# Performance work log

Hardware: AMD Instinct MI355X
Metric: run time of the kernel (lower is better)

## Reference

```python
import jax, jax.numpy as jnp
import numpy as np

S, I, C_M, C_P, C_Z = 128, 384, 256, 32, 128

def setup_inputs() -> dict:
    key = jax.random.key(0)
    ks = jax.random.split(key, 7)
    sc = 1.0 / np.sqrt(C_M)
    return {
        "msa_rep": jax.random.normal(ks[0], (S, I, C_M), jnp.float32),
        "ln_gamma": jnp.ones((C_M,), jnp.float32),
        "ln_beta": jnp.zeros((C_M,), jnp.float32),
        "Wa": jax.random.normal(ks[1], (C_P, C_M), jnp.float32) * sc,
        "Wb": jax.random.normal(ks[2], (C_P, C_M), jnp.float32) * sc,
        "Wproj": jax.random.normal(ks[3], (C_Z, C_P * C_P), jnp.float32) / np.sqrt(C_P * C_P),
        "bproj": jnp.zeros((C_Z,), jnp.float32),
    }

def reference(msa_rep, ln_gamma, ln_beta, Wa, Wb, Wproj, bproj):
    # LayerNorm over last dim (eps matches torch default 1e-5)
    mu = jnp.mean(msa_rep, axis=-1, keepdims=True)
    var = jnp.mean(jnp.square(msa_rep - mu), axis=-1, keepdims=True)
    x = (msa_rep - mu) * jax.lax.rsqrt(var + 1e-5) * ln_gamma + ln_beta
    # Two linear projections (torch Linear: y = x @ W.T), no bias
    a = jnp.einsum('sic,pc->sip', x, Wa)  # [s, i, c_p]
    b = jnp.einsum('sic,pc->sip', x, Wb)  # [s, i, c_p]
    norm = 1.0 / msa_rep.shape[-3]
    # Outer product mean over sequences s -> [i, j, c, d]
    outer = norm * jnp.einsum('sic,sjd->ijcd', a, b)
    outer = outer.reshape(outer.shape[0], outer.shape[1], -1)  # [i, j, c*c]
    return jnp.einsum('ijk,zk->ijz', outer, Wproj) + bproj  # [i, j, c_z]
```

## Files before the change

### kernel.cpp

```cpp
#include <hip/hip_runtime.h>
#include <hip/hip_bf16.h>

typedef short s8v  __attribute__((ext_vector_type(8)));
typedef float f32x4 __attribute__((ext_vector_type(4)));

__device__ __forceinline__ unsigned short f2bf(float f) {
  unsigned int b = __float_as_uint(f);
  b += 0x7fffu + ((b >> 16) & 1u);
  return (unsigned short)(b >> 16);
}

__global__ __launch_bounds__(256) void prep_w_kernel(
    const float* __restrict__ Wa, const float* __restrict__ Wb,
    const float* __restrict__ Wproj,
    unsigned short* __restrict__ wab, unsigned short* __restrict__ wfrag) {
  int gid = blockIdx.x * 256 + threadIdx.x;
  if (gid < 16384) {
    int e = gid;
    int j = e & 7, lane = (e >> 3) & 63, kt = (e >> 9) & 7, nt = e >> 12;
    int p = nt * 16 + (lane & 15);
    int c = kt * 32 + ((lane >> 4) << 3) + j;
    float v = (p < 32) ? Wa[p * 256 + c] : Wb[(p - 32) * 256 + c];
    wab[e] = f2bf(v);
  } else {
    int e = gid - 16384;
    int j = e & 7, lane = (e >> 3) & 63, kt = (e >> 9) & 31, nt = e >> 14;
    int z = nt * 16 + (lane & 15);
    int kp = kt * 32 + ((lane >> 4) << 3) + j;
    int c = kp & 31, d = kp >> 5;
    wfrag[e] = f2bf(Wproj[z * 1024 + c * 32 + d]);
  }
}

#define XS 264
#define OS 66
__global__ __launch_bounds__(256) void kernel_a(
    const float* __restrict__ msa, const float* __restrict__ gamma, const float* __restrict__ beta,
    const unsigned short* __restrict__ wab,
    unsigned short* __restrict__ afrag, unsigned short* __restrict__ bfrag) {
  __shared__ unsigned short xs[64 * XS];
  __shared__ float os[64 * OS];
  const int i  = blockIdx.x >> 1;
  const int sh = blockIdx.x & 1;
  const int tid = threadIdx.x;
  const int w = tid >> 6, lane = tid & 63;
  const int gq = lane >> 4, nlo = lane & 15;

  const float4 g4  = *(const float4*)(gamma + lane * 4);
  const float4 be4 = *(const float4*)(beta  + lane * 4);

  for (int it = 0; it < 16; ++it) {
    const int sl = it * 4 + w;
    const int s  = sh * 64 + sl;
    const float4 v = *(const float4*)(msa + (size_t)(s * 384 + i) * 256 + lane * 4);
    float sum = v.x + v.y + v.z + v.w;
    float sq  = fmaf(v.x, v.x, fmaf(v.y, v.y, fmaf(v.z, v.z, v.w * v.w)));
#pragma unroll
    for (int off = 32; off >= 1; off >>= 1) {
      sum += __shfl_xor(sum, off);
      sq  += __shfl_xor(sq,  off);
    }
    const float mu   = sum * (1.f / 256.f);
    const float var  = sq * (1.f / 256.f) - mu * mu;
    const float rstd = rsqrtf(var + 1e-5f);
    unsigned int lo = (unsigned int)f2bf((v.x - mu) * rstd * g4.x + be4.x)
                    | ((unsigned int)f2bf((v.y - mu) * rstd * g4.y + be4.y) << 16);
    unsigned int hi = (unsigned int)f2bf((v.z - mu) * rstd * g4.z + be4.z)
                    | ((unsigned int)f2bf((v.w - mu) * rstd * g4.w + be4.w) << 16);
    *(uint2*)&xs[sl * XS + lane * 4] = make_uint2(lo, hi);
  }
  __syncthreads();

  const f32x4 z4 = {0.f, 0.f, 0.f, 0.f};
  f32x4 acc[4];
#pragma unroll
  for (int nt = 0; nt < 4; ++nt) acc[nt] = z4;
  for (int kt = 0; kt < 8; ++kt) {
    const s8v av = *(const s8v*)&xs[(w * 16 + nlo) * XS + kt * 32 + gq * 8];
#pragma unroll
    for (int nt = 0; nt < 4; ++nt) {
      const s8v bv = ((const s8v*)wab)[(nt * 8 + kt) * 64 + lane];
      acc[nt] = __builtin_amdgcn_mfma_f32_16x16x32_bf16(av, bv, acc[nt], 0, 0, 0);
    }
  }
#pragma unroll
  for (int nt = 0; nt < 4; ++nt)
#pragma unroll
    for (int r = 0; r < 4; ++r)
      os[(w * 16 + gq * 4 + r) * OS + nt * 16 + nlo] = acc[nt][r];
  __syncthreads();

#pragma unroll
  for (int q = 0; q < 2; ++q) {
    const int set = q * 256 + tid;
    const int lf  = set & 63;
    const int ktl = (set >> 6) & 1;
    const int hi2 = (set >> 7) & 1;
    const int mat = (set >> 8) & 1;
    const int g2  = lf >> 4;
    const int p   = mat * 32 + (lf & 15) + 16 * hi2;
    s8v pk;
#pragma unroll
    for (int j = 0; j < 8; ++j) {
      const int srow = ktl * 32 + g2 * 8 + j;
      pk[j] = (short)f2bf(os[srow * OS + p]);
    }
    unsigned short* dst = mat ? bfrag : afrag;
    const int rb = i * 2 + hi2;
    const int kt = sh * 2 + ktl;
    *(s8v*)(dst + ((size_t)((rb * 4 + kt) * 64 + lf)) * 8) = pk;
  }
}

#define TS 1032
__global__ __launch_bounds__(512, 2) void kernel_main(
    const unsigned short* __restrict__ afrag, const unsigned short* __restrict__ bfrag,
    const unsigned short* __restrict__ wfrag, const float* __restrict__ bproj,
    float* __restrict__ out) {
  extern __shared__ unsigned short t[];
  const int bid = blockIdx.x;
  const int bi = bid / 48, bj = bid % 48;
  const int tid = threadIdx.x;
  const int wave = tid >> 6, lane = tid & 63;
  const int wm = wave >> 1, wn = wave & 1;
  const int gq = lane >> 4, nlo = lane & 15;

  const f32x4 z4 = {0.f, 0.f, 0.f, 0.f};
  f32x4 acc[4][8];
#pragma unroll
  for (int mt = 0; mt < 4; ++mt)
#pragma unroll
    for (int nt = 0; nt < 8; ++nt) acc[mt][nt] = z4;

  const s8v* ag = (const s8v*)afrag;
  const s8v* bg = (const s8v*)bfrag;
#pragma unroll
  for (int kt = 0; kt < 4; ++kt) {
    s8v av[4], bv[8];
#pragma unroll
    for (int mt = 0; mt < 4; ++mt)
      av[mt] = ag[((bi * 16 + wm * 4 + mt) * 4 + kt) * 64 + lane];
#pragma unroll
    for (int nt = 0; nt < 8; ++nt)
      bv[nt] = bg[((bj * 16 + wn * 8 + nt) * 4 + kt) * 64 + lane];
#pragma unroll
    for (int mt = 0; mt < 4; ++mt)
#pragma unroll
      for (int nt = 0; nt < 8; ++nt)
        acc[mt][nt] = __builtin_amdgcn_mfma_f32_16x16x32_bf16(av[mt], bv[nt], acc[mt][nt], 0, 0, 0);
  }

#pragma unroll
  for (int mt = 0; mt < 4; ++mt) {
    const int m0 = wm * 64 + mt * 16 + gq * 4;
    const int iloc = m0 >> 5;
    const int c0 = m0 & 31;
#pragma unroll
    for (int nt = 0; nt < 8; ++nt) {
      const int n = wn * 128 + nt * 16 + nlo;
      const int jloc = n >> 5, d = n & 31;
      const int ij = iloc * 8 + jloc;
      const unsigned int lo = (unsigned int)f2bf(acc[mt][nt][0] * 0.0078125f)
                            | ((unsigned int)f2bf(acc[mt][nt][1] * 0.0078125f) << 16);
      const unsigned int hi = (unsigned int)f2bf(acc[mt][nt][2] * 0.0078125f)
                            | ((unsigned int)f2bf(acc[mt][nt][3] * 0.0078125f) << 16);
      const int off = (d * 32 + c0) ^ ((d & 3) << 3);
      *(uint2*)&t[ij * TS + off] = make_uint2(lo, hi);
    }
  }
  __syncthreads();

  const float bz = bproj[wave * 16 + nlo];
  f32x4 acc2[4];
#pragma unroll
  for (int mt = 0; mt < 4; ++mt) acc2[mt] = z4;
  const s8v* wg = (const s8v*)wfrag;
  for (int kt2 = 0; kt2 < 32; ++kt2) {
    const s8v wv = wg[(wave * 32 + kt2) * 64 + lane];
    const int roff = (kt2 * 32 + gq * 8) ^ ((kt2 & 3) << 3);
#pragma unroll
    for (int mt = 0; mt < 4; ++mt) {
      const s8v av2 = *(const s8v*)&t[(mt * 16 + nlo) * TS + roff];
      acc2[mt] = __builtin_amdgcn_mfma_f32_16x16x32_bf16(av2, wv, acc2[mt], 0, 0, 0);
    }
  }

  const int z = wave * 16 + nlo;
#pragma unroll
  for (int mt = 0; mt < 4; ++mt)
#pragma unroll
    for (int r = 0; r < 4; ++r) {
      const int ijl = mt * 16 + gq * 4 + r;
      const int gi = bi * 8 + (ijl >> 3), gj = bj * 8 + (ijl & 7);
      out[(size_t)(gi * 384 + gj) * 128 + z] = acc2[mt][r] + bz;
    }
}

extern "C" void kernel_launch(void* const* d_in, const int* in_sizes, int n_in,
                              void* d_out, int out_size, void* d_ws, size_t ws_size,
                              hipStream_t stream) {
  const float* msa   = (const float*)d_in[0];
  const float* gam   = (const float*)d_in[1];
  const float* bet   = (const float*)d_in[2];
  const float* Wa    = (const float*)d_in[3];
  const float* Wb    = (const float*)d_in[4];
  const float* Wproj = (const float*)d_in[5];
  const float* bpr   = (const float*)d_in[6];
  float* out = (float*)d_out;

  if (ws_size < 6586368) return;
  unsigned short* afrag = (unsigned short*)d_ws;
  unsigned short* bfrag = afrag + 1572864;
  unsigned short* wab   = bfrag + 1572864;
  unsigned short* wfr   = wab + 16384;

  (void)hipFuncSetAttribute(reinterpret_cast<const void*>(kernel_main),
                            hipFuncAttributeMaxDynamicSharedMemorySize, 64 * TS * 2);

  prep_w_kernel<<<576, 256, 0, stream>>>(Wa, Wb, Wproj, wab, wfr);
  kernel_a<<<768, 256, 0, stream>>>(msa, gam, bet, wab, afrag, bfrag);
  kernel_main<<<2304, 512, 64 * TS * 2, stream>>>(afrag, bfrag, wfr, bpr, out);
}
```

Baseline: 125.2 us.

## Split main kernel into d-chunks to halve LDS and registers, raise occupancy

The fused outer-product plus projection kernel now computes the outer product in two halves over the d dimension, staging each half into a half-size LDS tile and accumulating the projection GEMM across the chunks. This cuts the live accumulator count and the LDS footprint so four blocks can fit per CU instead of two, aiming to hide memory latency better. Block IDs are also remapped with a stride to change the order tiles are scheduled across the chip. The cost is extra synchronisations, reloading the A fragments for each chunk, and a new LDS swizzle.

New measurement: 149.2 us. 19.2% more time.

```diff
diff --git a/kernel.cpp b/kernel.cpp
--- a/kernel.cpp
+++ b/kernel.cpp
@@ -112,86 +112,92 @@
   }
 }
 
-#define TS 1032
-__global__ __launch_bounds__(512, 2) void kernel_main(
+#define TS5 520
+__global__ __launch_bounds__(512, 4) void kernel_main(
     const unsigned short* __restrict__ afrag, const unsigned short* __restrict__ bfrag,
     const unsigned short* __restrict__ wfrag, const float* __restrict__ bproj,
     float* __restrict__ out) {
   extern __shared__ unsigned short t[];
-  const int bid = blockIdx.x;
+  const int bid = (blockIdx.x & 7) * 288 + (blockIdx.x >> 3);
   const int bi = bid / 48, bj = bid % 48;
   const int tid = threadIdx.x;
   const int wave = tid >> 6, lane = tid & 63;
   const int wm = wave >> 1, wn = wave & 1;
   const int gq = lane >> 4, nlo = lane & 15;
 
-  const f32x4 z4 = {0.f, 0.f, 0.f, 0.f};
-  f32x4 acc[4][8];
-#pragma unroll
-  for (int mt = 0; mt < 4; ++mt)
-#pragma unroll
-    for (int nt = 0; nt < 8; ++nt) acc[mt][nt] = z4;
-
   const s8v* ag = (const s8v*)afrag;
   const s8v* bg = (const s8v*)bfrag;
-#pragma unroll
-  for (int kt = 0; kt < 4; ++kt) {
-    s8v av[4], bv[8];
-#pragma unroll
-    for (int mt = 0; mt < 4; ++mt)
-      av[mt] = ag[((bi * 16 + wm * 4 + mt) * 4 + kt) * 64 + lane];
-#pragma unroll
-    for (int nt = 0; nt < 8; ++nt)
-      bv[nt] = bg[((bj * 16 + wn * 8 + nt) * 4 + kt) * 64 + lane];
-#pragma unroll
-    for (int mt = 0; mt < 4; ++mt)
-#pragma unroll
-      for (int nt = 0; nt < 8; ++nt)
-        acc[mt][nt] = __builtin_amdgcn_mfma_f32_16x16x32_bf16(av[mt], bv[nt], acc[mt][nt], 0, 0, 0);
-  }
-
-#pragma unroll
-  for (int mt = 0; mt < 4; ++mt) {
-    const int m0 = wm * 64 + mt * 16 + gq * 4;
-    const int iloc = m0 >> 5;
-    const int c0 = m0 & 31;
-#pragma unroll
-    for (int nt = 0; nt < 8; ++nt) {
-      const int n = wn * 128 + nt * 16 + nlo;
-      const int jloc = n >> 5, d = n & 31;
-      const int ij = iloc * 8 + jloc;
-      const unsigned int lo = (unsigned int)f2bf(acc[mt][nt][0] * 0.0078125f)
-                            | ((unsigned int)f2bf(acc[mt][nt][1] * 0.0078125f) << 16);
-      const unsigned int hi = (unsigned int)f2bf(acc[mt][nt][2] * 0.0078125f)
-                            | ((unsigned int)f2bf(acc[mt][nt][3] * 0.0078125f) << 16);
-      const int off = (d * 32 + c0) ^ ((d & 3) << 3);
-      *(uint2*)&t[ij * TS + off] = make_uint2(lo, hi);
-    }
-  }
-  __syncthreads();
-
-  const float bz = bproj[wave * 16 + nlo];
+  const s8v* wg = (const s8v*)wfrag;
+  const f32x4 z4 = {0.f, 0.f, 0.f, 0.f};
+
   f32x4 acc2[4];
 #pragma unroll
   for (int mt = 0; mt < 4; ++mt) acc2[mt] = z4;
-  const s8v* wg = (const s8v*)wfrag;
-  for (int kt2 = 0; kt2 < 32; ++kt2) {
-    const s8v wv = wg[(wave * 32 + kt2) * 64 + lane];
-    const int roff = (kt2 * 32 + gq * 8) ^ ((kt2 & 3) << 3);
-#pragma unroll
-    for (int mt = 0; mt < 4; ++mt) {
-      const s8v av2 = *(const s8v*)&t[(mt * 16 + nlo) * TS + roff];
-      acc2[mt] = __builtin_amdgcn_mfma_f32_16x16x32_bf16(av2, wv, acc2[mt], 0, 0, 0);
-    }
+
+#pragma unroll 1
+  for (int dc = 0; dc < 2; ++dc) {
+#pragma unroll 1
+    for (int ph = 0; ph < 2; ++ph) {
+      f32x4 acc[4][2];
+#pragma unroll
+      for (int mt = 0; mt < 4; ++mt) { acc[mt][0] = z4; acc[mt][1] = z4; }
+#pragma unroll 2
+      for (int kt = 0; kt < 4; ++kt) {
+        s8v av[4];
+#pragma unroll
+        for (int mt = 0; mt < 4; ++mt)
+          av[mt] = ag[((bi * 16 + wm * 4 + mt) * 4 + kt) * 64 + lane];
+        s8v bv[2];
+#pragma unroll
+        for (int nt = 0; nt < 2; ++nt)
+          bv[nt] = bg[(((bj * 8 + ph * 4 + wn * 2 + nt) * 2 + dc) * 4 + kt) * 64 + lane];
+#pragma unroll
+        for (int mt = 0; mt < 4; ++mt)
+#pragma unroll
+          for (int nt = 0; nt < 2; ++nt)
+            acc[mt][nt] = __builtin_amdgcn_mfma_f32_16x16x32_bf16(av[mt], bv[nt], acc[mt][nt], 0, 0, 0);
+      }
+      if (dc && ph == 0) __syncthreads();
+#pragma unroll
+      for (int mt = 0; mt < 4; ++mt) {
+        const int row0 = (wm * 2 + (mt >> 1)) * 8 + ph * 4 + wn * 2;
+        const int c0 = (mt & 1) * 16 + 4 * gq;
+        const int hw = nlo * 32 + (c0 ^ (8 * ((nlo >> 1) & 3)));
+#pragma unroll
+        for (int nt = 0; nt < 2; ++nt) {
+          const unsigned int lo = (unsigned int)f2bf(acc[mt][nt][0] * 0.0078125f)
+                                | ((unsigned int)f2bf(acc[mt][nt][1] * 0.0078125f) << 16);
+          const unsigned int hi = (unsigned int)f2bf(acc[mt][nt][2] * 0.0078125f)
+                                | ((unsigned int)f2bf(acc[mt][nt][3] * 0.0078125f) << 16);
+          *(uint2*)&t[(row0 + nt) * TS5 + hw] = make_uint2(lo, hi);
+        }
+      }
+    }
+    __syncthreads();
+
+#pragma unroll 2
+    for (int kt2 = 0; kt2 < 16; ++kt2) {
+      const int hwb = kt2 * 32 + 8 * (gq ^ ((kt2 >> 1) & 3));
+      const s8v wv = wg[(wave * 32 + dc * 16 + kt2) * 64 + lane];
+      s8v av2[4];
+#pragma unroll
+      for (int mt = 0; mt < 4; ++mt)
+        av2[mt] = *(const s8v*)&t[(mt * 16 + nlo) * TS5 + hwb];
+#pragma unroll
+      for (int mt = 0; mt < 4; ++mt)
+        acc2[mt] = __builtin_amdgcn_mfma_f32_16x16x32_bf16(av2[mt], wv, acc2[mt], 0, 0, 0);
+    }
+    if (!dc) __syncthreads();
   }
 
   const int z = wave * 16 + nlo;
+  const float bz = bproj[z];
 #pragma unroll
   for (int mt = 0; mt < 4; ++mt)
 #pragma unroll
     for (int r = 0; r < 4; ++r) {
-      const int ijl = mt * 16 + gq * 4 + r;
-      const int gi = bi * 8 + (ijl >> 3), gj = bj * 8 + (ijl & 7);
+      const int ij = mt * 16 + gq * 4 + r;
+      const int gi = bi * 8 + (ij >> 3), gj = bj * 8 + (ij & 7);
       out[(size_t)(gi * 384 + gj) * 128 + z] = acc2[mt][r] + bz;
     }
 }
@@ -215,9 +221,9 @@
   unsigned short* wfr   = wab + 16384;
 
   (void)hipFuncSetAttribute(reinterpret_cast<const void*>(kernel_main),
-                            hipFuncAttributeMaxDynamicSharedMemorySize, 64 * TS * 2);
+                            hipFuncAttributeMaxDynamicSharedMemorySize, 64 * TS5 * 2);
 
   prep_w_kernel<<<576, 256, 0, stream>>>(Wa, Wb, Wproj, wab, wfr);
   kernel_a<<<768, 256, 0, stream>>>(msa, gam, bet, wab, afrag, bfrag);
-  kernel_main<<<2304, 512, 64 * TS * 2, stream>>>(afrag, bfrag, wfr, bpr, out);
-}
+  kernel_main<<<2304, 512, 64 * TS5 * 2, stream>>>(afrag, bfrag, wfr, bpr, out);
+}
```
